# Performance work log

Measured on AMD Instinct MI355X. Metric: run time of the kernel, lower is better.

Reference implementation:

```python
import jax, jax.numpy as jnp
import numpy as np

NU, N1, N2 = 100000, 60000, 60000   # users, domain-1 items, domain-2 items
E = 2000000                          # click edges per domain
DIN, DH, DOUT = 128, 128, 64


def setup_inputs() -> dict:
    key = jax.random.key(0)
    ks = jax.random.split(key, 14)
    emb = lambda k, shape: jax.random.normal(k, shape, dtype=jnp.float32) * 0.01
    w = lambda k, shape: jax.random.normal(k, shape, dtype=jnp.float32) * (1.0 / np.sqrt(shape[-2]))
    return {
        "emb_user": emb(ks[0], (NU, DIN)),
        "emb_d1": emb(ks[1], (N1, DIN)),
        "emb_d2": emb(ks[2], (N2, DIN)),
        # relation order: [user->d1 click, d1->user rev, user->d2 click, d2->user rev]
        "W_in": w(ks[3], (4, DIN, DH)),
        "b_in": jnp.zeros((4, DH), jnp.float32),
        "W_hid": w(ks[4], (4, DH, DH)),
        "b_hid": jnp.zeros((4, DH), jnp.float32),
        "W_out": w(ks[5], (4, DH, DOUT)),
        "b_out": jnp.zeros((4, DOUT), jnp.float32),
        "Wp_d1": jax.random.normal(ks[6], (DOUT, DOUT), dtype=jnp.float32),
        "Wp_d2": jax.random.normal(ks[7], (DOUT, DOUT), dtype=jnp.float32),
        "src_d1": jax.random.randint(ks[8], (E,), 0, NU, dtype=jnp.int32),
        "dst_d1": jax.random.randint(ks[9], (E,), 0, N1, dtype=jnp.int32),
        "src_d2": jax.random.randint(ks[10], (E,), 0, NU, dtype=jnp.int32),
        "dst_d2": jax.random.randint(ks[11], (E,), 0, N2, dtype=jnp.int32),
    }


def _gconv(x_src, W, b, src, dst, nsrc, ndst, n_dst):
    # DGL GraphConv, norm='both': D_dst^{-1/2} A D_src^{-1/2} (X W) + b
    m = (x_src * nsrc[:, None]) @ W                      # [N_src, dout]
    agg = jax.ops.segment_sum(m[src], dst, num_segments=n_dst)  # SpMM via gather/scatter
    return agg * ndst[:, None] + b


def reference(emb_user, emb_d1, emb_d2, W_in, b_in, W_hid, b_hid, W_out, b_out,
              Wp_d1, Wp_d2, src_d1, dst_d1, src_d2, dst_d2):
    Nu, Na, Nb = emb_user.shape[0], emb_d1.shape[0], emb_d2.shape[0]
    ones1 = jnp.ones(src_d1.shape[0], jnp.float32)
    ones2 = jnp.ones(src_d2.shape[0], jnp.float32)
    du1 = jax.ops.segment_sum(ones1, src_d1, num_segments=Nu)
    di1 = jax.ops.segment_sum(ones1, dst_d1, num_segments=Na)
    du2 = jax.ops.segment_sum(ones2, src_d2, num_segments=Nu)
    di2 = jax.ops.segment_sum(ones2, dst_d2, num_segments=Nb)
    r = lambda d: jax.lax.rsqrt(jnp.maximum(d, 1.0))
    nu1, ni1, nu2, ni2 = r(du1), r(di1), r(du2), r(di2)

    u, i1, i2 = emb_user, emb_d1, emb_d2
    layers = ((W_in, b_in, False), (W_hid, b_hid, False), (W_out, b_out, True))
    for W, b, last in layers:
        # HeteroGraphConv with aggregate='sum': user receives from both reverse relations
        u_new = (_gconv(i1, W[1], b[1], dst_d1, src_d1, ni1, nu1, Nu)
                 + _gconv(i2, W[3], b[3], dst_d2, src_d2, ni2, nu2, Nu))
        i1_new = _gconv(u, W[0], b[0], src_d1, dst_d1, nu1, ni1, Na)
        i2_new = _gconv(u, W[2], b[2], src_d2, dst_d2, nu2, ni2, Nb)
        if last:
            u, i1, i2 = u_new, i1_new, i2_new
        else:  # relu + dropout (eval mode: dropout is identity)
            u, i1, i2 = jax.nn.relu(u_new), jax.nn.relu(i1_new), jax.nn.relu(i2_new)

    # per-domain projection of user embeddings, then u_dot_v edge scoring
    u1 = u @ Wp_d1
    u2 = u @ Wp_d2
    s1 = jnp.sum(u1[src_d1] * i1[dst_d1], axis=-1)  # [E]
    s2 = jnp.sum(u2[src_d2] * i2[dst_d2], axis=-1)  # [E]
    return jnp.concatenate([s1, s2])
```

## Files before the change

### kernel.cpp

```cpp
#include <hip/hip_runtime.h>
#include <hip/hip_bf16.h>

typedef unsigned short ushort_t;
typedef __attribute__((ext_vector_type(8))) short bf16x8;
typedef __attribute__((ext_vector_type(4))) float f32x4;

constexpr int NU = 100000, N1 = 60000, N2 = 60000;
constexpr int E = 2000000;
constexpr int TOTN = 2 * NU + N1 + N2;
constexpr int NPART = 8;
constexpr int CH = 2048;
constexpr int NCHUNKS = (E + CH - 1) / CH;
constexpr int PSLICE = TOTN / NPART;
constexpr int NSUB = 8;
constexpr int SUBS = PSLICE / NSUB;
constexpr int CH2 = 8192;
constexpr int NCH2 = (E + CH2 - 1) / CH2;
constexpr int NSUB2 = 4;
constexpr int SUBS2 = PSLICE / NSUB2;

__device__ __forceinline__ ushort_t f2bf(float f) {
  unsigned u = __float_as_uint(f);
  u = u + 0x7fffu + ((u >> 16) & 1u);
  return (ushort_t)(u >> 16);
}
__device__ __forceinline__ float bf2f(ushort_t v) {
  return __uint_as_float(((unsigned)v) << 16);
}

__global__ __launch_bounds__(256) void k_count(const int* __restrict__ s1,
                                               const int* __restrict__ d1,
                                               const int* __restrict__ s2,
                                               const int* __restrict__ d2,
                                               int* __restrict__ deg) {
  __shared__ int ls1[CH], ld1[CH], ls2[CH], ld2[CH];
  int part = blockIdx.x % NPART;
  int base = (blockIdx.x / NPART) * CH;
  int n = E - base; if (n > CH) n = CH;
  for (int i = threadIdx.x; i < n; i += 256) {
    ls1[i] = s1[base + i];
    ld1[i] = d1[base + i];
    ls2[i] = s2[base + i];
    ld2[i] = d2[base + i];
  }
  __syncthreads();
  int plo = part * PSLICE;
  for (int sub = 0; sub < NSUB; ++sub) {
    int lo = plo + sub * SUBS, hi = lo + SUBS;
    for (int i = threadIdx.x; i < n; i += 256) {
      int i0 = ls1[i];
      int i1 = NU + ld1[i];
      int i2 = NU + N1 + ls2[i];
      int i3 = 2 * NU + N1 + ld2[i];
      if (i0 >= lo && i0 < hi) atomicAdd(&deg[i0], 1);
      if (i1 >= lo && i1 < hi) atomicAdd(&deg[i1], 1);
      if (i2 >= lo && i2 < hi) atomicAdd(&deg[i2], 1);
      if (i3 >= lo && i3 < hi) atomicAdd(&deg[i3], 1);
    }
    __syncthreads();
  }
}

__global__ __launch_bounds__(256) void k_norm(const int* __restrict__ deg,
                                              float* __restrict__ nrm) {
  int i = blockIdx.x * 256 + threadIdx.x;
  if (i >= TOTN) return;
  int d = deg[i];
  nrm[i] = rsqrtf((float)(d > 1 ? d : 1));
}

__global__ __launch_bounds__(256) void k_scan(const int* __restrict__ deg,
                                              int* __restrict__ off,
                                              int* __restrict__ cur) {
  __shared__ int wsum[4];
  int seg = blockIdx.x;
  int baseIn, n, baseOut;
  if (seg == 0)      { baseIn = 0;            n = NU; baseOut = 0; }
  else if (seg == 1) { baseIn = NU;           n = N1; baseOut = NU + 1; }
  else if (seg == 2) { baseIn = NU + N1;      n = NU; baseOut = NU + N1 + 2; }
  else               { baseIn = 2 * NU + N1;  n = N2; baseOut = 2 * NU + N1 + 3; }
  const int* in = deg + baseIn;
  int* out = off + baseOut;
  int* curp = cur + baseIn;

  constexpr int ITEMS = 16;
  int t = threadIdx.x, lane = t & 63, wid = t >> 6;
  int carry = 0;
  for (int base = 0; base < n; base += 256 * ITEMS) {
    int vals[ITEMS];
    int lsum = 0;
    int i0 = base + t * ITEMS;
#pragma unroll
    for (int j = 0; j < ITEMS; ++j) {
      int i = i0 + j;
      int v = (i < n) ? in[i] : 0;
      vals[j] = v;
      lsum += v;
    }
    int incl = lsum;
#pragma unroll
    for (int d = 1; d < 64; d <<= 1) {
      int x = __shfl_up(incl, d, 64);
      if (lane >= d) incl += x;
    }
    if (lane == 63) wsum[wid] = incl;
    __syncthreads();
    int woff = 0;
    for (int w = 0; w < wid; ++w) woff += wsum[w];
    int chunkTotal = wsum[0] + wsum[1] + wsum[2] + wsum[3];
    int excl = carry + woff + (incl - lsum);
#pragma unroll
    for (int j = 0; j < ITEMS; ++j) {
      int i = i0 + j;
      if (i < n) { out[i] = excl; curp[i] = excl; }
      excl += vals[j];
    }
    carry += chunkTotal;
    __syncthreads();
  }
  if (t == 0) out[n] = carry;
}

__global__ __launch_bounds__(256) void k_fill2(const int* __restrict__ s1,
                                               const int* __restrict__ d1,
                                               const int* __restrict__ s2,
                                               const int* __restrict__ d2,
                                               int* __restrict__ cur,
                                               int2* __restrict__ ae_s1,
                                               int* __restrict__ a_d1,
                                               int2* __restrict__ ae_s2,
                                               int* __restrict__ a_d2) {
  int part = blockIdx.x % NPART;
  int chunk = (blockIdx.x / NPART) % NCH2;
  int sub = blockIdx.x / (NPART * NCH2);
  int lo = part * PSLICE + sub * SUBS2, hi = lo + SUBS2;
  int base = chunk * CH2;
  int end = base + CH2 < E ? base + CH2 : E;
  for (int i = base + threadIdx.x; i < end; i += 256) {
    int a = s1[i], b = d1[i];
    if (a >= lo && a < hi) {
      int pos = atomicAdd(&cur[a], 1);
      ae_s1[pos] = make_int2(b, i);
    }
    int i1 = NU + b;
    if (i1 >= lo && i1 < hi) a_d1[atomicAdd(&cur[i1], 1)] = a;
    int c = s2[i], d = d2[i];
    int i2 = NU + N1 + c;
    if (i2 >= lo && i2 < hi) {
      int pos = atomicAdd(&cur[i2], 1);
      ae_s2[pos] = make_int2(d, i);
    }
    int i3 = 2 * NU + N1 + d;
    if (i3 >= lo && i3 < hi) a_d2[atomicAdd(&cur[i3], 1)] = c;
  }
}

__device__ __forceinline__ bf16x8 loadA8(const float* p) {
  float4 lo = *(const float4*)p;
  float4 hi = *(const float4*)(p + 4);
  bf16x8 v;
  v[0] = (short)f2bf(lo.x); v[1] = (short)f2bf(lo.y);
  v[2] = (short)f2bf(lo.z); v[3] = (short)f2bf(lo.w);
  v[4] = (short)f2bf(hi.x); v[5] = (short)f2bf(hi.y);
  v[6] = (short)f2bf(hi.z); v[7] = (short)f2bf(hi.w);
  return v;
}
__device__ __forceinline__ bf16x8 loadA8(const ushort_t* p) {
  return *(const bf16x8*)p;
}

template <typename AT, int K, int N, bool BF16OUT>
__global__ __launch_bounds__(256) void k_gemm(const AT* __restrict__ A,
                                              const float* __restrict__ W,
                                              void* __restrict__ Cv, int M,
                                              const float* __restrict__ rowscale) {
  constexpr int KF = K / 32, NF = N / 16;
  __shared__ __align__(16) ushort_t sW[N * K];
  for (int i = threadIdx.x * 4; i < K * N; i += 1024) {
    float4 w4 = *(const float4*)&W[i];
    int k = i / N, n0 = i % N;
    float wv[4] = {w4.x, w4.y, w4.z, w4.w};
#pragma unroll
    for (int j = 0; j < 4; ++j) {
      int n = n0 + j;
      sW[(n * K + k) ^ ((n & 7) << 3)] = f2bf(wv[j]);
    }
  }
  __syncthreads();

  int w = threadIdx.x >> 6, lane = threadIdx.x & 63;
  int col = lane & 15, kg = lane >> 4;
  int r = blockIdx.x * 64 + w * 16 + col;
  int rA = r < M ? r : M - 1;

  bf16x8 af[KF];
#pragma unroll
  for (int kf = 0; kf < KF; ++kf)
    af[kf] = loadA8(&A[(size_t)rA * K + kf * 32 + kg * 8]);

  f32x4 acc[NF] = {};
#pragma unroll
  for (int nf = 0; nf < NF; ++nf) {
    int n = nf * 16 + col;
#pragma unroll
    for (int kf = 0; kf < KF; ++kf) {
      int idx = (n * K + kf * 32 + kg * 8) ^ ((n & 7) << 3);
      bf16x8 bfrag = *(const bf16x8*)&sW[idx];
      acc[nf] = __builtin_amdgcn_mfma_f32_16x16x32_bf16(af[kf], bfrag, acc[nf], 0, 0, 0);
    }
  }

  int orow = blockIdx.x * 64 + w * 16 + kg * 4;
#pragma unroll
  for (int reg = 0; reg < 4; ++reg) {
    int R = orow + reg;
    if (R >= M) break;
    float sc = rowscale ? rowscale[R] : 1.f;
#pragma unroll
    for (int nf = 0; nf < NF; ++nf) {
      float v = sc * acc[nf][reg];
      size_t o = (size_t)R * N + nf * 16 + col;
      if constexpr (BF16OUT) ((ushort_t*)Cv)[o] = f2bf(v);
      else                   ((float*)Cv)[o] = v;
    }
  }
}

__device__ __forceinline__ int adj_idx(int v) { return v; }
__device__ __forceinline__ int adj_idx(int2 v) { return v.x; }

template <int D, typename IdxT>
__device__ __forceinline__ void accum_list(const ushort_t* __restrict__ z,
                                           const IdxT* __restrict__ adj,
                                           int e0, int e1, int l, float4& A) {
  auto addp = [&](uint2 p) {
    A.x += __uint_as_float(p.x << 16);
    A.y += __uint_as_float(p.x & 0xffff0000u);
    A.z += __uint_as_float(p.y << 16);
    A.w += __uint_as_float(p.y & 0xffff0000u);
  };
  int e = e0;
  for (; e + 8 <= e1; e += 8) {
    uint2 p[8];
#pragma unroll
    for (int j = 0; j < 8; ++j)
      p[j] = *(const uint2*)&z[(size_t)adj_idx(adj[e + j]) * D + 4 * l];
#pragma unroll
    for (int j = 0; j < 8; ++j) addp(p[j]);
  }
  for (; e < e1; ++e)
    addp(*(const uint2*)&z[(size_t)adj_idx(adj[e]) * D + 4 * l]);
}

template <int D, bool RELU, bool BF16OUT>
__global__ __launch_bounds__(256) void k_gather(const ushort_t* __restrict__ z,
                                                const int* __restrict__ off,
                                                const int* __restrict__ adj,
                                                const float* __restrict__ ndst,
                                                const float* __restrict__ bias,
                                                void* __restrict__ outv, int nv) {
  constexpr int LPN = D / 4;
  constexpr int NPB = 256 / LPN;
  int t = threadIdx.x;
  int slot = t / LPN, l = t % LPN;
  int v = blockIdx.x * NPB + slot;
  if (v >= nv) return;
  float4 A = {0.f, 0.f, 0.f, 0.f};
  accum_list<D>(z, adj, off[v], off[v + 1], l, A);
  float nd = ndst[v];
  float r0 = nd * A.x + bias[4 * l];
  float r1 = nd * A.y + bias[4 * l + 1];
  float r2 = nd * A.z + bias[4 * l + 2];
  float r3 = nd * A.w + bias[4 * l + 3];
  if constexpr (RELU) {
    r0 = fmaxf(r0, 0.f); r1 = fmaxf(r1, 0.f);
    r2 = fmaxf(r2, 0.f); r3 = fmaxf(r3, 0.f);
  }
  size_t o = (size_t)v * D + 4 * l;
  if constexpr (BF16OUT) {
    uint2 pk;
    pk.x = (unsigned)f2bf(r0) | ((unsigned)f2bf(r1) << 16);
    pk.y = (unsigned)f2bf(r2) | ((unsigned)f2bf(r3) << 16);
    *(uint2*)&((ushort_t*)outv)[o] = pk;
  } else {
    float4 res; res.x = r0; res.y = r1; res.z = r2; res.w = r3;
    *(float4*)&((float*)outv)[o] = res;
  }
}

template <int D, bool RELU>
__global__ __launch_bounds__(256) void k_gather2(const ushort_t* __restrict__ z1,
                                                 const ushort_t* __restrict__ z2,
                                                 const int* __restrict__ off1,
                                                 const int2* __restrict__ ae1,
                                                 const int* __restrict__ off2,
                                                 const int2* __restrict__ ae2,
                                                 const float* __restrict__ nd1,
                                                 const float* __restrict__ nd2,
                                                 const float* __restrict__ b1,
                                                 const float* __restrict__ b2,
                                                 ushort_t* __restrict__ out, int nv) {
  constexpr int LPN = D / 4;
  constexpr int NPB = 256 / LPN;
  int t = threadIdx.x;
  int slot = t / LPN, l = t % LPN;
  int v = blockIdx.x * NPB + slot;
  if (v >= nv) return;
  float4 A = {0.f, 0.f, 0.f, 0.f};
  float4 B = {0.f, 0.f, 0.f, 0.f};
  accum_list<D>(z1, ae1, off1[v], off1[v + 1], l, A);
  accum_list<D>(z2, ae2, off2[v], off2[v + 1], l, B);
  float n1 = nd1[v], n2 = nd2[v];
  float r0 = n1 * A.x + n2 * B.x + b1[4 * l]     + b2[4 * l];
  float r1 = n1 * A.y + n2 * B.y + b1[4 * l + 1] + b2[4 * l + 1];
  float r2 = n1 * A.z + n2 * B.z + b1[4 * l + 2] + b2[4 * l + 2];
  float r3 = n1 * A.w + n2 * B.w + b1[4 * l + 3] + b2[4 * l + 3];
  if constexpr (RELU) {
    r0 = fmaxf(r0, 0.f); r1 = fmaxf(r1, 0.f);
    r2 = fmaxf(r2, 0.f); r3 = fmaxf(r3, 0.f);
  }
  uint2 pk;
  pk.x = (unsigned)f2bf(r0) | ((unsigned)f2bf(r1) << 16);
  pk.y = (unsigned)f2bf(r2) | ((unsigned)f2bf(r3) << 16);
  *(uint2*)&out[(size_t)v * D + 4 * l] = pk;
}

__global__ __launch_bounds__(256) void k_score2(const ushort_t* __restrict__ u64,
                                                const float* __restrict__ Wp,
                                                const float* __restrict__ ip,
                                                const int* __restrict__ off,
                                                const int2* __restrict__ ae,
                                                float* __restrict__ out, int nu) {
  __shared__ float sWp[64 * 64];
  for (int i = threadIdx.x * 4; i < 4096; i += 1024)
    *(float4*)&sWp[i] = *(const float4*)&Wp[i];
  __syncthreads();
  int w = threadIdx.x >> 6, lane = threadIdx.x & 63;
  int u = blockIdx.x * 4 + w;
  if (u >= nu) return;
  float x = bf2f(u64[(size_t)u * 64 + lane]);
  float p = 0.f;
#pragma unroll
  for (int c = 0; c < 64; ++c) {
    float xc = __shfl(x, c, 64);
    p += xc * sWp[c * 64 + lane];
  }
  int e0 = off[u], e1 = off[u + 1];
  int e = e0;
  for (; e + 2 <= e1; e += 2) {
    int2 A = ae[e], B = ae[e + 1];
    float pA = p * ip[(size_t)A.x * 64 + lane];
    float pB = p * ip[(size_t)B.x * 64 + lane];
#pragma unroll
    for (int d = 32; d >= 1; d >>= 1) {
      pA += __shfl_xor(pA, d, 64);
      pB += __shfl_xor(pB, d, 64);
    }
    if (lane == 0) { out[A.y] = pA; out[B.y] = pB; }
  }
  if (e < e1) {
    int2 A = ae[e];
    float pA = p * ip[(size_t)A.x * 64 + lane];
#pragma unroll
    for (int d = 32; d >= 1; d >>= 1) pA += __shfl_xor(pA, d, 64);
    if (lane == 0) out[A.y] = pA;
  }
}

extern "C" void kernel_launch(void* const* d_in, const int* in_sizes, int n_in,
                              void* d_out, int out_size, void* d_ws, size_t ws_size,
                              hipStream_t stream) {
  const float* emb_user = (const float*)d_in[0];
  const float* emb_d1   = (const float*)d_in[1];
  const float* emb_d2   = (const float*)d_in[2];
  const float* W_in     = (const float*)d_in[3];
  const float* b_in     = (const float*)d_in[4];
  const float* W_hid    = (const float*)d_in[5];
  const float* b_hid    = (const float*)d_in[6];
  const float* W_out    = (const float*)d_in[7];
  const float* b_out    = (const float*)d_in[8];
  const float* Wp_d1    = (const float*)d_in[9];
  const float* Wp_d2    = (const float*)d_in[10];
  const int* src_d1     = (const int*)d_in[11];
  const int* dst_d1     = (const int*)d_in[12];
  const int* src_d2     = (const int*)d_in[13];
  const int* dst_d2     = (const int*)d_in[14];
  float* out = (float*)d_out;

  char* p = (char*)d_ws;
  auto alloc = [&](size_t bytes) {
    void* r = (void*)p;
    p += (bytes + 15) & ~(size_t)15;
    return r;
  };
  ushort_t* bufU[2] = {(ushort_t*)alloc((size_t)NU * 128 * 2),
                       (ushort_t*)alloc((size_t)NU * 128 * 2)};
  void* bufI1 = alloc((size_t)N1 * 128 * 2);
  void* bufI2 = alloc((size_t)N2 * 128 * 2);
  ushort_t* m = (ushort_t*)alloc((size_t)(N1 + N2) * 128 * 2);
  float* nrm = (float*)alloc((size_t)TOTN * 4);
  int* deg = (int*)alloc((size_t)TOTN * 4);
  int* off = (int*)alloc((size_t)(TOTN + 4) * 4);
  int* cur = (int*)alloc((size_t)TOTN * 4);
  int2* ae_s1 = (int2*)alloc((size_t)E * 8);
  int* adj_d1 = (int*)alloc((size_t)E * 4);
  int2* ae_s2 = (int2*)alloc((size_t)E * 8);
  int* adj_d2 = (int*)alloc((size_t)E * 4);

  if ((size_t)(p - (char*)d_ws) > ws_size) return;

  const float* nu1 = nrm;
  const float* ni1 = nrm + NU;
  const float* nu2 = nrm + NU + N1;
  const float* ni2 = nrm + 2 * NU + N1;
  const int* off_u1 = off;
  const int* off_i1 = off + NU + 1;
  const int* off_u2 = off + NU + N1 + 2;
  const int* off_i2 = off + 2 * NU + N1 + 3;

  hipMemsetAsync(deg, 0, (size_t)TOTN * 4, stream);
  k_count<<<NCHUNKS * NPART, 256, 0, stream>>>(src_d1, dst_d1, src_d2, dst_d2, deg);
  k_norm<<<(TOTN + 255) / 256, 256, 0, stream>>>(deg, nrm);
  k_scan<<<4, 256, 0, stream>>>(deg, off, cur);
  k_fill2<<<NSUB2 * NCH2 * NPART, 256, 0, stream>>>(src_d1, dst_d1, src_d2, dst_d2, cur,
                                                    ae_s1, adj_d1, ae_s2, adj_d2);

  ushort_t* mI1 = m;
  ushort_t* mI2 = m + (size_t)N1 * 128;
  ushort_t* mI1h = m;
  ushort_t* mI2h = m + (size_t)N1 * 64;
  ushort_t* mU = m;

  k_gemm<float, 128, 128, true><<<(N1 + 63) / 64, 256, 0, stream>>>(emb_d1, W_in + 1 * 128 * 128, mI1, N1, ni1);
  k_gemm<float, 128, 128, true><<<(N2 + 63) / 64, 256, 0, stream>>>(emb_d2, W_in + 3 * 128 * 128, mI2, N2, ni2);
  k_gather2<128, true><<<(NU + 7) / 8, 256, 0, stream>>>(
      mI1, mI2, off_u1, ae_s1, off_u2, ae_s2, nu1, nu2,
      b_in + 1 * 128, b_in + 3 * 128, bufU[0], NU);
  k_gemm<float, 128, 128, true><<<(NU + 63) / 64, 256, 0, stream>>>(emb_user, W_in + 0 * 128 * 128, mU, NU, nu1);
  k_gather<128, true, true><<<(N1 + 7) / 8, 256, 0, stream>>>(
      mU, off_i1, adj_d1, ni1, b_in + 0 * 128, bufI1, N1);
  k_gemm<float, 128, 128, true><<<(NU + 63) / 64, 256, 0, stream>>>(emb_user, W_in + 2 * 128 * 128, mU, NU, nu2);
  k_gather<128, true, true><<<(N2 + 7) / 8, 256, 0, stream>>>(
      mU, off_i2, adj_d2, ni2, b_in + 2 * 128, bufI2, N2);

  k_gemm<ushort_t, 128, 128, true><<<(N1 + 63) / 64, 256, 0, stream>>>((ushort_t*)bufI1, W_hid + 1 * 128 * 128, mI1, N1, ni1);
  k_gemm<ushort_t, 128, 128, true><<<(N2 + 63) / 64, 256, 0, stream>>>((ushort_t*)bufI2, W_hid + 3 * 128 * 128, mI2, N2, ni2);
  k_gather2<128, true><<<(NU + 7) / 8, 256, 0, stream>>>(
      mI1, mI2, off_u1, ae_s1, off_u2, ae_s2, nu1, nu2,
      b_hid + 1 * 128, b_hid + 3 * 128, bufU[1], NU);
  k_gemm<ushort_t, 128, 128, true><<<(NU + 63) / 64, 256, 0, stream>>>(bufU[0], W_hid + 0 * 128 * 128, mU, NU, nu1);
  k_gather<128, true, true><<<(N1 + 7) / 8, 256, 0, stream>>>(
      mU, off_i1, adj_d1, ni1, b_hid + 0 * 128, bufI1, N1);
  k_gemm<ushort_t, 128, 128, true><<<(NU + 63) / 64, 256, 0, stream>>>(bufU[0], W_hid + 2 * 128 * 128, mU, NU, nu2);
  k_gather<128, true, true><<<(N2 + 7) / 8, 256, 0, stream>>>(
      mU, off_i2, adj_d2, ni2, b_hid + 2 * 128, bufI2, N2);

  k_gemm<ushort_t, 128, 64, true><<<(N1 + 63) / 64, 256, 0, stream>>>((ushort_t*)bufI1, W_out + 1 * 128 * 64, mI1h, N1, ni1);
  k_gemm<ushort_t, 128, 64, true><<<(N2 + 63) / 64, 256, 0, stream>>>((ushort_t*)bufI2, W_out + 3 * 128 * 64, mI2h, N2, ni2);
  k_gather2<64, false><<<(NU + 15) / 16, 256, 0, stream>>>(
      mI1h, mI2h, off_u1, ae_s1, off_u2, ae_s2, nu1, nu2,
      b_out + 1 * 64, b_out + 3 * 64, bufU[0], NU);
  k_gemm<ushort_t, 128, 64, true><<<(NU + 63) / 64, 256, 0, stream>>>(bufU[1], W_out + 0 * 128 * 64, mU, NU, nu1);
  k_gather<64, false, false><<<(N1 + 15) / 16, 256, 0, stream>>>(
      mU, off_i1, adj_d1, ni1, b_out + 0 * 64, bufI1, N1);
  k_gemm<ushort_t, 128, 64, true><<<(NU + 63) / 64, 256, 0, stream>>>(bufU[1], W_out + 2 * 128 * 64, mU, NU, nu2);
  k_gather<64, false, false><<<(N2 + 15) / 16, 256, 0, stream>>>(
      mU, off_i2, adj_d2, ni2, b_out + 2 * 64, bufI2, N2);

  k_score2<<<(NU + 3) / 4, 256, 0, stream>>>(bufU[0], Wp_d1, (const float*)bufI1,
                                             off_u1, ae_s1, out, NU);
  k_score2<<<(NU + 3) / 4, 256, 0, stream>>>(bufU[0], Wp_d2, (const float*)bufI2,
                                             off_u2, ae_s2, out + E, NU);
}
```

Measured before the change: 2.470 ms.

## Replace partitioned CSR fill with two-pass LDS bucketing then per-bucket scatter

Replaces the multi-pass partitioned CSR fill, which rescanned every edge once per node partition, with a two-level bucketing scheme. Edges are first binned into 64 coarse node buckets using shared-memory staging and packed 64/32-bit entries written to reused scratch buffers. A second kernel then scatters each bucket's edges into their final CSR slots, so the atomics and writes stay localized. This cuts redundant edge reads but adds extra kernels and a temporary round trip, and it relies on bit-packing limits on node and edge index widths.

```diff
diff --git a/kernel.cpp b/kernel.cpp
--- a/kernel.cpp
+++ b/kernel.cpp
@@ -2,6 +2,7 @@
 #include <hip/hip_bf16.h>
 
 typedef unsigned short ushort_t;
+typedef unsigned long long u64_t;
 typedef __attribute__((ext_vector_type(8))) short bf16x8;
 typedef __attribute__((ext_vector_type(4))) float f32x4;
 
@@ -14,10 +15,12 @@
 constexpr int PSLICE = TOTN / NPART;
 constexpr int NSUB = 8;
 constexpr int SUBS = PSLICE / NSUB;
-constexpr int CH2 = 8192;
-constexpr int NCH2 = (E + CH2 - 1) / CH2;
-constexpr int NSUB2 = 4;
-constexpr int SUBS2 = PSLICE / NSUB2;
+constexpr int NB = 64;
+constexpr int BS_U = (NU + NB - 1) / NB;
+constexpr int BS_I = (N1 + NB - 1) / NB;
+constexpr int CAPA = 72;
+constexpr int CHA = 2048;
+constexpr int NBLKA = (E + CHA - 1) / CHA;
 
 __device__ __forceinline__ ushort_t f2bf(float f) {
   unsigned u = __float_as_uint(f);
@@ -121,37 +124,121 @@
   if (t == 0) out[n] = carry;
 }
 
-__global__ __launch_bounds__(256) void k_fill2(const int* __restrict__ s1,
-                                               const int* __restrict__ d1,
-                                               const int* __restrict__ s2,
-                                               const int* __restrict__ d2,
-                                               int* __restrict__ cur,
-                                               int2* __restrict__ ae_s1,
-                                               int* __restrict__ a_d1,
-                                               int2* __restrict__ ae_s2,
-                                               int* __restrict__ a_d2) {
-  int part = blockIdx.x % NPART;
-  int chunk = (blockIdx.x / NPART) % NCH2;
-  int sub = blockIdx.x / (NPART * NCH2);
-  int lo = part * PSLICE + sub * SUBS2, hi = lo + SUBS2;
-  int base = chunk * CH2;
-  int end = base + CH2 < E ? base + CH2 : E;
-  for (int i = base + threadIdx.x; i < end; i += 256) {
-    int a = s1[i], b = d1[i];
-    if (a >= lo && a < hi) {
-      int pos = atomicAdd(&cur[a], 1);
-      ae_s1[pos] = make_int2(b, i);
-    }
-    int i1 = NU + b;
-    if (i1 >= lo && i1 < hi) a_d1[atomicAdd(&cur[i1], 1)] = a;
-    int c = s2[i], d = d2[i];
-    int i2 = NU + N1 + c;
-    if (i2 >= lo && i2 < hi) {
-      int pos = atomicAdd(&cur[i2], 1);
-      ae_s2[pos] = make_int2(d, i);
-    }
-    int i3 = 2 * NU + N1 + d;
-    if (i3 >= lo && i3 < hi) a_d2[atomicAdd(&cur[i3], 1)] = c;
+__global__ void k_binit(const int* __restrict__ off, int* __restrict__ gcur) {
+  int t = threadIdx.x;
+  int l = t >> 6, b = t & 63;
+  const int* offl; int n, bs;
+  if (l == 0)      { offl = off;                 n = NU; bs = BS_U; }
+  else if (l == 1) { offl = off + NU + 1;        n = N1; bs = BS_I; }
+  else if (l == 2) { offl = off + NU + N1 + 2;   n = NU; bs = BS_U; }
+  else             { offl = off + 2*NU + N1 + 3; n = N2; bs = BS_I; }
+  int lo = b * bs; if (lo > n) lo = n;
+  gcur[t] = offl[lo];
+}
+
+__global__ __launch_bounds__(256) void k_bucketU(const int* __restrict__ nd,
+                                                 const int* __restrict__ pl,
+                                                 int* __restrict__ gcur,
+                                                 u64_t* __restrict__ tmp) {
+  __shared__ u64_t buf[NB][CAPA];
+  __shared__ int cnt[NB];
+  int t = threadIdx.x, lane = t & 63, wid = t >> 6;
+  if (t < NB) cnt[t] = 0;
+  __syncthreads();
+  int base = blockIdx.x * CHA;
+  int end = base + CHA < E ? base + CHA : E;
+  for (int i = base + t; i < end; i += 256) {
+    int node = nd[i];
+    int b = node / BS_U;
+    u64_t en = (u64_t)(node - b * BS_U) | ((u64_t)pl[i] << 11) | ((u64_t)i << 27);
+    int pos = atomicAdd(&cnt[b], 1);
+    if (pos < CAPA) buf[b][pos] = en;
+    else tmp[atomicAdd(&gcur[b], 1)] = en;
+  }
+  __syncthreads();
+  for (int b = wid; b < NB; b += 4) {
+    int cb = cnt[b]; if (cb > CAPA) cb = CAPA;
+    int gbase = 0;
+    if (lane == 0) gbase = atomicAdd(&gcur[b], cb);
+    gbase = __shfl(gbase, 0, 64);
+    for (int i = lane; i < cb; i += 64) tmp[gbase + i] = buf[b][i];
+  }
+}
+
+__global__ __launch_bounds__(256) void k_bucketI(const int* __restrict__ nd,
+                                                 const int* __restrict__ pl,
+                                                 int* __restrict__ gcur,
+                                                 unsigned* __restrict__ tmp) {
+  __shared__ unsigned buf[NB][CAPA];
+  __shared__ int cnt[NB];
+  int t = threadIdx.x, lane = t & 63, wid = t >> 6;
+  if (t < NB) cnt[t] = 0;
+  __syncthreads();
+  int base = blockIdx.x * CHA;
+  int end = base + CHA < E ? base + CHA : E;
+  for (int i = base + t; i < end; i += 256) {
+    int node = nd[i];
+    int b = node / BS_I;
+    unsigned en = (unsigned)(node - b * BS_I) | ((unsigned)pl[i] << 10);
+    int pos = atomicAdd(&cnt[b], 1);
+    if (pos < CAPA) buf[b][pos] = en;
+    else tmp[atomicAdd(&gcur[b], 1)] = en;
+  }
+  __syncthreads();
+  for (int b = wid; b < NB; b += 4) {
+    int cb = cnt[b]; if (cb > CAPA) cb = CAPA;
+    int gbase = 0;
+    if (lane == 0) gbase = atomicAdd(&gcur[b], cb);
+    gbase = __shfl(gbase, 0, 64);
+    for (int i = lane; i < cb; i += 64) tmp[gbase + i] = buf[b][i];
+  }
+}
+
+__global__ __launch_bounds__(256) void k_scatterB(const u64_t* __restrict__ t_s1,
+                                                  const unsigned* __restrict__ t_d1,
+                                                  const u64_t* __restrict__ t_s2,
+                                                  const unsigned* __restrict__ t_d2,
+                                                  const int* __restrict__ off,
+                                                  int* __restrict__ cur,
+                                                  int2* __restrict__ ae_s1,
+                                                  int* __restrict__ a_d1,
+                                                  int2* __restrict__ ae_s2,
+                                                  int* __restrict__ a_d2) {
+  int l = blockIdx.x >> 6, b = blockIdx.x & 63;
+  int t = threadIdx.x;
+  if (l == 0 || l == 2) {
+    const u64_t* tmp = (l == 0) ? t_s1 : t_s2;
+    const int* offl = (l == 0) ? off : off + NU + N1 + 2;
+    int curb = (l == 0) ? 0 : NU + N1;
+    int2* ae = (l == 0) ? ae_s1 : ae_s2;
+    int blo = b * BS_U, bhi = blo + BS_U;
+    if (blo > NU) blo = NU;
+    if (bhi > NU) bhi = NU;
+    int s = offl[blo], e = offl[bhi];
+    for (int i = s + t; i < e; i += 256) {
+      u64_t en = tmp[i];
+      int local = (int)(en & 2047u);
+      int item = (int)((en >> 11) & 0xFFFFu);
+      int eid = (int)(en >> 27);
+      int pos = atomicAdd(&cur[curb + blo + local], 1);
+      ae[pos] = make_int2(item, eid);
+    }
+  } else {
+    const unsigned* tmp = (l == 1) ? t_d1 : t_d2;
+    const int* offl = (l == 1) ? off + NU + 1 : off + 2 * NU + N1 + 3;
+    int curb = (l == 1) ? NU : 2 * NU + N1;
+    int* adj = (l == 1) ? a_d1 : a_d2;
+    int blo = b * BS_I, bhi = blo + BS_I;
+    if (blo > N1) blo = N1;
+    if (bhi > N1) bhi = N1;
+    int s = offl[blo], e = offl[bhi];
+    for (int i = s + t; i < e; i += 256) {
+      unsigned en = tmp[i];
+      int local = (int)(en & 1023u);
+      int user = (int)(en >> 10);
+      int pos = atomicAdd(&cur[curb + blo + local], 1);
+      adj[pos] = user;
+    }
   }
 }
 
@@ -325,7 +412,7 @@
   *(uint2*)&out[(size_t)v * D + 4 * l] = pk;
 }
 
-__global__ __launch_bounds__(256) void k_score2(const ushort_t* __restrict__ u64,
+__global__ __launch_bounds__(256) void k_score2(const ushort_t* __restrict__ u64v,
                                                 const float* __restrict__ Wp,
                                                 const float* __restrict__ ip,
                                                 const int* __restrict__ off,
@@ -338,7 +425,7 @@
   int w = threadIdx.x >> 6, lane = threadIdx.x & 63;
   int u = blockIdx.x * 4 + w;
   if (u >= nu) return;
-  float x = bf2f(u64[(size_t)u * 64 + lane]);
+  float x = bf2f(u64v[(size_t)u * 64 + lane]);
   float p = 0.f;
 #pragma unroll
   for (int c = 0; c < 64; ++c) {
@@ -406,6 +493,12 @@
   int* adj_d1 = (int*)alloc((size_t)E * 4);
   int2* ae_s2 = (int2*)alloc((size_t)E * 8);
   int* adj_d2 = (int*)alloc((size_t)E * 4);
+  int* gcur = (int*)alloc(4 * NB * 4);
+
+  u64_t* t_s1 = (u64_t*)bufU[0];
+  u64_t* t_s2 = (u64_t*)bufU[1];
+  unsigned* t_d1 = (unsigned*)m;
+  unsigned* t_d2 = (unsigned*)((char*)m + (size_t)E * 4);
 
   if ((size_t)(p - (char*)d_ws) > ws_size) return;
 
@@ -422,8 +515,13 @@
   k_count<<<NCHUNKS * NPART, 256, 0, stream>>>(src_d1, dst_d1, src_d2, dst_d2, deg);
   k_norm<<<(TOTN + 255) / 256, 256, 0, stream>>>(deg, nrm);
   k_scan<<<4, 256, 0, stream>>>(deg, off, cur);
-  k_fill2<<<NSUB2 * NCH2 * NPART, 256, 0, stream>>>(src_d1, dst_d1, src_d2, dst_d2, cur,
-                                                    ae_s1, adj_d1, ae_s2, adj_d2);
+  k_binit<<<1, 256, 0, stream>>>(off, gcur);
+  k_bucketU<<<NBLKA, 256, 0, stream>>>(src_d1, dst_d1, gcur + 0 * NB, t_s1);
+  k_bucketI<<<NBLKA, 256, 0, stream>>>(dst_d1, src_d1, gcur + 1 * NB, t_d1);
+  k_bucketU<<<NBLKA, 256, 0, stream>>>(src_d2, dst_d2, gcur + 2 * NB, t_s2);
+  k_bucketI<<<NBLKA, 256, 0, stream>>>(dst_d2, src_d2, gcur + 3 * NB, t_d2);
+  k_scatterB<<<4 * NB, 256, 0, stream>>>(t_s1, t_d1, t_s2, t_d2, off, cur,
+                                         ae_s1, adj_d1, ae_s2, adj_d2);
 
   ushort_t* mI1 = m;
   ushort_t* mI2 = m + (size_t)N1 * 128;
```

New measurement: 4.692 ms. 1.9x slower.
